# Performance work log

Measured on AMD Instinct MI355X. Metric: run time of the kernel, lower is better.

The kernel has to match this reference:

```python
import jax, jax.numpy as jnp
import numpy as np

EPS = 1e-6
N_HEADS = 16
N_KV_HEADS = 4
HEAD_DIM = 128
DIM = 2048
SEQ = 2048
BATCH = 2


def _make_freqs_cis(seqlen, head_dim, theta=10000.0):
    inv = 1.0 / (theta ** (jnp.arange(0, head_dim, 2, dtype=jnp.float32) / head_dim))  # [hd/2]
    t = jnp.arange(seqlen, dtype=jnp.float32)
    ang = jnp.outer(t, inv)  # [seq, hd/2]
    return jnp.stack([jnp.cos(ang), jnp.sin(ang)], axis=-1)  # [seq, hd/2, 2]


def setup_inputs() -> dict:
    key = jax.random.key(0)
    k1, k2, k3 = jax.random.split(key, 3)
    std = 0.02
    x = jax.random.normal(k1, (BATCH, SEQ, DIM), dtype=jnp.float32)
    freqs_cis = _make_freqs_cis(SEQ, HEAD_DIM)
    norm_w = jnp.ones((DIM,), dtype=jnp.float32)
    wqkv_w = jax.random.normal(k2, ((N_HEADS + 2 * N_KV_HEADS) * HEAD_DIM, DIM), dtype=jnp.float32) * std
    wo_w = jax.random.normal(k3, (DIM, N_HEADS * HEAD_DIM), dtype=jnp.float32) * std
    return {"x": x, "freqs_cis": freqs_cis, "norm_w": norm_w, "wqkv_w": wqkv_w, "wo_w": wo_w}


def _rope(t, cos, sin):
    # t: [b, s, h, hd] viewed as pairs; cos/sin: [s, hd/2]
    b, s, h, hd = t.shape
    tr = t.reshape(b, s, h, hd // 2, 2)
    xr, xi = tr[..., 0], tr[..., 1]
    c = cos[None, :, None, :]
    sn = sin[None, :, None, :]
    out_r = xr * c - xi * sn
    out_i = xr * sn + xi * c
    return jnp.stack([out_r, out_i], axis=-1).reshape(b, s, h, hd)


def reference(x, freqs_cis, norm_w, wqkv_w, wo_w):
    bs, seqlen, dim = x.shape
    n_rep = N_HEADS // N_KV_HEADS
    # RMSNorm
    xn = x * jax.lax.rsqrt(jnp.mean(x * x, axis=-1, keepdims=True) + EPS) * norm_w
    # fused QKV projection
    qkv = jnp.einsum('bsd,ed->bse', xn, wqkv_w)
    q_sz = N_HEADS * HEAD_DIM
    kv_sz = N_KV_HEADS * HEAD_DIM
    xq = qkv[..., :q_sz].reshape(bs, seqlen, N_HEADS, HEAD_DIM)
    xk = qkv[..., q_sz:q_sz + kv_sz].reshape(bs, seqlen, N_KV_HEADS, HEAD_DIM)
    xv = qkv[..., q_sz + kv_sz:].reshape(bs, seqlen, N_KV_HEADS, HEAD_DIM)
    cos, sin = freqs_cis[..., 0], freqs_cis[..., 1]
    xq = _rope(xq, cos, sin)
    xk = _rope(xk, cos, sin)
    # GQA: group q heads so kv broadcast replaces repeat_kv materialization
    q = xq.transpose(0, 2, 1, 3).reshape(bs, N_KV_HEADS, n_rep, seqlen, HEAD_DIM)
    k = xk.transpose(0, 2, 1, 3)  # [b, g, s, d]
    v = xv.transpose(0, 2, 1, 3)
    scale = 1.0 / jnp.sqrt(jnp.float32(HEAD_DIM))
    scores = jnp.einsum('bgrqd,bgkd->bgrqk', q, k) * scale
    causal = jnp.tril(jnp.ones((seqlen, seqlen), dtype=bool))
    scores = jnp.where(causal, scores, jnp.finfo(scores.dtype).min)
    probs = jax.nn.softmax(scores, axis=-1)
    out = jnp.einsum('bgrqk,bgkd->bgrqd', probs, v)
    out = out.reshape(bs, N_HEADS, seqlen, HEAD_DIM).transpose(0, 2, 1, 3).reshape(bs, seqlen, N_HEADS * HEAD_DIM)
    return jnp.einsum('bse,de->bsd', out, wo_w)
```

## Files before the change

### kernel.cpp

```cpp
#include <hip/hip_runtime.h>
#include <cstdint>
#include <cstddef>

typedef __bf16 bhalf;
typedef __bf16 bhalf8 __attribute__((ext_vector_type(8)));
typedef __bf16 bhalf4 __attribute__((ext_vector_type(4)));
typedef float f32x4 __attribute__((ext_vector_type(4)));
typedef float f32x16 __attribute__((ext_vector_type(16)));

#define RMS_EPS 1e-6f
#define N_HEADS 16
#define N_KV 4
#define HD 128
#define DIM 2048
#define SEQ 2048
#define BATCH 2

static __device__ __forceinline__ f32x4 mfma16(bhalf8 a, bhalf8 b, f32x4 c) {
    return __builtin_amdgcn_mfma_f32_16x16x32_bf16(a, b, c, 0, 0, 0);
}
static __device__ __forceinline__ f32x16 mfma32(bhalf8 a, bhalf8 b, f32x16 c) {
    return __builtin_amdgcn_mfma_f32_32x32x16_bf16(a, b, c, 0, 0, 0);
}

static __device__ __forceinline__ void gload16(const bhalf* g, bhalf* l) {
    __builtin_amdgcn_global_load_lds((const __attribute__((address_space(1))) unsigned int*)g,
                                     (__attribute__((address_space(3))) unsigned int*)l,
                                     16, 0, 0);
}

static __device__ __forceinline__ unsigned cvt_pk_bf16(float a, float b) {
    unsigned r;
    asm volatile("v_cvt_pk_bf16_f32 %0, %1, %2" : "=v"(r) : "v"(a), "v"(b));
    return r;
}
static __device__ __forceinline__ void plane32_swap(unsigned& a, unsigned& b) {
    asm volatile("v_permlane32_swap_b32 %0, %1" : "+v"(a), "+v"(b));
}

__global__ __launch_bounds__(256) void cvt_w(const float* __restrict__ a,
                                             const float* __restrict__ b,
                                             bhalf* __restrict__ dst) {
    size_t i = ((size_t)blockIdx.x * 256 + threadIdx.x) * 4;
    const size_t NQ = (size_t)3072 * 2048;
    float4 v = (i < NQ) ? ((const float4*)a)[i >> 2] : ((const float4*)b)[(i - NQ) >> 2];
    bhalf4 o;
    o[0] = (bhalf)v.x; o[1] = (bhalf)v.y; o[2] = (bhalf)v.z; o[3] = (bhalf)v.w;
    *(bhalf4*)(dst + i) = o;
}

__global__ __launch_bounds__(256) void rmsnorm_k(const float* __restrict__ x,
                                                 const float* __restrict__ w,
                                                 bhalf* __restrict__ xn) {
    const int row = blockIdx.x;
    const int tid = threadIdx.x;
    const float4* xr = (const float4*)(x + (size_t)row * DIM);
    float4 v0 = xr[tid * 2], v1 = xr[tid * 2 + 1];
    float ss = v0.x * v0.x + v0.y * v0.y + v0.z * v0.z + v0.w * v0.w
             + v1.x * v1.x + v1.y * v1.y + v1.z * v1.z + v1.w * v1.w;
    #pragma unroll
    for (int off = 32; off; off >>= 1) ss += __shfl_xor(ss, off, 64);
    __shared__ float red[4];
    if ((tid & 63) == 0) red[tid >> 6] = ss;
    __syncthreads();
    float tot = red[0] + red[1] + red[2] + red[3];
    float scale = rsqrtf(tot * (1.0f / DIM) + RMS_EPS);
    const float4* wr = (const float4*)w;
    float4 w0 = wr[tid * 2], w1 = wr[tid * 2 + 1];
    bhalf8 o;
    o[0] = (bhalf)(v0.x * scale * w0.x); o[1] = (bhalf)(v0.y * scale * w0.y);
    o[2] = (bhalf)(v0.z * scale * w0.z); o[3] = (bhalf)(v0.w * scale * w0.w);
    o[4] = (bhalf)(v1.x * scale * w1.x); o[5] = (bhalf)(v1.y * scale * w1.y);
    o[6] = (bhalf)(v1.z * scale * w1.z); o[7] = (bhalf)(v1.w * scale * w1.w);
    *(bhalf8*)(xn + (size_t)row * DIM + tid * 8) = o;
}

template <typename OutT>
__global__ __launch_bounds__(512) void gemm256(const bhalf* __restrict__ A,
                                               const bhalf* __restrict__ B,
                                               OutT* __restrict__ C,
                                               int N, int K) {
    extern __shared__ __align__(16) char smem[];
    const int tid = threadIdx.x;
    const int wid = tid >> 6, lane = tid & 63;
    const int quad = lane >> 4, r16 = lane & 15;
    const int wm = wid >> 2, wn = wid & 3;

    const int nx = N >> 8;
    const int cpx = (int)gridDim.x >> 3;
    const int bs = (int)blockIdx.x;
    const int bid = (bs & 7) * cpx + (bs >> 3);
    const int m0 = (bid / nx) << 8, n0 = (bid % nx) << 8;

    const int srow = wid * 32 + (lane >> 2);
    const int scol = ((lane & 3) ^ ((lane >> 2) & 3)) << 3;
    const bhalf* Ast = A + (size_t)(m0 + srow) * K + scol;
    const bhalf* Bst = B + (size_t)(n0 + srow) * K + scol;
    const size_t r16K = (size_t)16 * K;

    const int xorr = (r16 & 3) << 4;
    const int rdA = (wm * 128 + r16) * 64 + ((quad * 16) ^ xorr);
    const int rdB = (wn * 64 + r16) * 64 + ((quad * 16) ^ xorr);

    char* const sA = smem;
    char* const sB = smem + 49152;

    f32x4 acc[8][4];
    #pragma unroll
    for (int i = 0; i < 8; ++i)
        #pragma unroll
        for (int j = 0; j < 4; ++j) acc[i][j] = (f32x4)0.0f;

    const int NT = K >> 5;

    #define STAGE256(P, bufbase, t) do {                                          \
        gload16((P) + (size_t)(t) * 32, (bhalf*)((bufbase) + wid * 2048));        \
        gload16((P) + (size_t)(t) * 32 + r16K, (bhalf*)((bufbase) + wid * 2048 + 1024)); \
    } while (0)

    STAGE256(Ast, sA, 0);
    STAGE256(Bst, sB, 0);
    STAGE256(Ast, sA + 16384, 1);
    STAGE256(Bst, sB + 16384, 1);
    asm volatile("s_waitcnt vmcnt(4)" ::: "memory");
    __builtin_amdgcn_s_barrier();

    int cur = 0, c2 = 2;
    for (int t = 0; t < NT; ++t) {
        char* const bufA = sA + cur * 16384;
        char* const bufB = sB + cur * 16384;
        bhalf8 bf[4], afl[4];
        #pragma unroll
        for (int j = 0; j < 4; ++j) bf[j] = *(const bhalf8*)(bufB + rdB + j * 1024);
        #pragma unroll
        for (int i = 0; i < 4; ++i) afl[i] = *(const bhalf8*)(bufA + rdA + i * 1024);
        if (t + 2 < NT) STAGE256(Ast, sA + c2 * 16384, t + 2);
        __builtin_amdgcn_s_barrier();
        __builtin_amdgcn_s_setprio(1);
        #pragma unroll
        for (int i = 0; i < 4; ++i)
            #pragma unroll
            for (int j = 0; j < 4; ++j)
                acc[i][j] = mfma16(afl[i], bf[j], acc[i][j]);
        __builtin_amdgcn_s_setprio(0);
        __builtin_amdgcn_s_barrier();
        bhalf8 afh[4];
        #pragma unroll
        for (int i = 0; i < 4; ++i) afh[i] = *(const bhalf8*)(bufA + rdA + 4096 + i * 1024);
        if (t + 2 < NT) STAGE256(Bst, sB + c2 * 16384, t + 2);
        asm volatile("s_waitcnt vmcnt(4)" ::: "memory");
        __builtin_amdgcn_s_barrier();
        __builtin_amdgcn_s_setprio(1);
        #pragma unroll
        for (int i = 0; i < 4; ++i)
            #pragma unroll
            for (int j = 0; j < 4; ++j)
                acc[i + 4][j] = mfma16(afh[i], bf[j], acc[i + 4][j]);
        __builtin_amdgcn_s_setprio(0);
        __builtin_amdgcn_s_barrier();
        cur = (cur == 2) ? 0 : cur + 1;
        c2 = (c2 == 2) ? 0 : c2 + 1;
    }
    #undef STAGE256

    #pragma unroll
    for (int i = 0; i < 8; ++i) {
        const int rbase = m0 + wm * 128 + i * 16 + quad * 4;
        #pragma unroll
        for (int rr = 0; rr < 4; ++rr) {
            OutT* crow = C + (size_t)(rbase + rr) * N + n0 + wn * 64 + r16;
            #pragma unroll
            for (int j = 0; j < 4; ++j) crow[j * 16] = (OutT)acc[i][j][rr];
        }
    }
}

__global__ __launch_bounds__(256) void rope_k(const bhalf* __restrict__ qkv,
                                              const float* __restrict__ freqs,
                                              bhalf* __restrict__ qb,
                                              bhalf* __restrict__ kb,
                                              bhalf* __restrict__ vt) {
    const int bs = blockIdx.x;
    const int b = bs >> 11, s = bs & 2047;
    const bhalf* row = qkv + (size_t)bs * 3072;
    const int tid = threadIdx.x;

    {
        const int h = tid >> 4, d20 = (tid & 15) * 4;
        bhalf8 e = *(const bhalf8*)(row + h * HD + d20 * 2);
        const float* fp = freqs + (size_t)s * 128 + d20 * 2;
        float4 f0 = *(const float4*)fp;
        float4 f1 = *(const float4*)(fp + 4);
        bhalf8 o;
        o[0] = (bhalf)((float)e[0] * f0.x - (float)e[1] * f0.y);
        o[1] = (bhalf)((float)e[0] * f0.y + (float)e[1] * f0.x);
        o[2] = (bhalf)((float)e[2] * f0.z - (float)e[3] * f0.w);
        o[3] = (bhalf)((float)e[2] * f0.w + (float)e[3] * f0.z);
        o[4] = (bhalf)((float)e[4] * f1.x - (float)e[5] * f1.y);
        o[5] = (bhalf)((float)e[4] * f1.y + (float)e[5] * f1.x);
        o[6] = (bhalf)((float)e[6] * f1.z - (float)e[7] * f1.w);
        o[7] = (bhalf)((float)e[6] * f1.w + (float)e[7] * f1.z);
        *(bhalf8*)(qb + ((size_t)(b * N_HEADS + h) * SEQ + s) * HD + d20 * 2) = o;
    }
    if (tid < 64) {
        const int kh = tid >> 4, d20 = (tid & 15) * 4;
        bhalf8 e = *(const bhalf8*)(row + 2048 + kh * HD + d20 * 2);
        const float* fp = freqs + (size_t)s * 128 + d20 * 2;
        float4 f0 = *(const float4*)fp;
        float4 f1 = *(const float4*)(fp + 4);
        bhalf8 o;
        o[0] = (bhalf)((float)e[0] * f0.x - (float)e[1] * f0.y);
        o[1] = (bhalf)((float)e[0] * f0.y + (float)e[1] * f0.x);
        o[2] = (bhalf)((float)e[2] * f0.z - (float)e[3] * f0.w);
        o[3] = (bhalf)((float)e[2] * f0.w + (float)e[3] * f0.z);
        o[4] = (bhalf)((float)e[4] * f1.x - (float)e[5] * f1.y);
        o[5] = (bhalf)((float)e[4] * f1.y + (float)e[5] * f1.x);
        o[6] = (bhalf)((float)e[6] * f1.z - (float)e[7] * f1.w);
        o[7] = (bhalf)((float)e[6] * f1.w + (float)e[7] * f1.z);
        *(bhalf8*)(kb + ((size_t)(b * N_KV + kh) * SEQ + s) * HD + d20 * 2) = o;
    }
    for (int e = tid; e < 512; e += 256) {
        const int kh = e >> 7, d = e & 127;
        vt[((size_t)(b * N_KV + kh) * HD + d) * SEQ + s] = row[2560 + e];
    }
}

__global__ __launch_bounds__(256, 2) void attn_k(const bhalf* __restrict__ qb,
                                                 const bhalf* __restrict__ kb,
                                                 const bhalf* __restrict__ vt,
                                                 bhalf* __restrict__ ob) {
    const int tid = threadIdx.x;
    const int wave = tid >> 6, lane = tid & 63;
    const int l31 = lane & 31, h2 = lane >> 5;
    const int qw = wave & 1, kw = wave >> 1;
    const int bid = ((blockIdx.x & 7) << 6) | ((int)blockIdx.x >> 3);
    const int pair = bid & 15;
    const int hh = (bid >> 4) & 15;
    const int b = bid >> 8;
    const int kvh = hh >> 2;

    __shared__ __align__(16) char smem[33792];
    char* const sK = smem;
    char* const sV = smem + 16384;
    float* const mrg = (float*)smem;

    const bhalf* Kbase = kb + (size_t)(b * N_KV + kvh) * SEQ * HD;
    const bhalf* Vbase = vt + (size_t)(b * N_KV + kvh) * HD * SEQ;
    const float SCL2 = 0.08838834764831845f * 1.4426950408889634f;

    const int mbase = (qw * 64 + lane) * 66;
    const int kr = tid >> 4, kce = (tid & 15) * 8;
    const int vr = tid >> 3, vce = (tid & 7) * 8;
    const int kcB = kce * 2, vcB = vce * 2;
    const int Xl = (h2 << 4) ^ ((l31 & 7) << 4);

    for (int phase = 0; phase < 2; ++phase) {
        const int qt = phase ? (31 - pair) : pair;
        const int qrow = qt * 64 + qw * 32 + l31;
        const int qhi = qt * 64 + qw * 32 + 31;

        const bhalf* qbase = qb + (((size_t)(b * N_HEADS + hh) * SEQ) + qrow) * HD;
        bhalf8 qf[8];
        #pragma unroll
        for (int kk = 0; kk < 8; ++kk) {
            bhalf8 q0 = *(const bhalf8*)(qbase + kk * 16 + h2 * 8);
            #pragma unroll
            for (int e = 0; e < 8; ++e) q0[e] = (bhalf)((float)q0[e] * SCL2);
            qf[kk] = q0;
        }

        f32x16 accO[4];
        #pragma unroll
        for (int dt = 0; dt < 4; ++dt) accO[dt] = (f32x16)0.0f;
        float m_i = -1e30f, l_i = 0.0f;

        bhalf8 kreg[4], vreg[4];
        #pragma unroll
        for (int i = 0; i < 4; ++i) {
            kreg[i] = *(const bhalf8*)(Kbase + (size_t)(kr + 16 * i) * HD + kce);
            vreg[i] = *(const bhalf8*)(Vbase + (size_t)(vr + 32 * i) * SEQ + vce);
        }

        for (int kt = 0; kt <= qt; ++kt) {
            __syncthreads();
            #pragma unroll
            for (int i = 0; i < 4; ++i) {
                const int rk = kr + 16 * i;
                *(bhalf8*)(sK + rk * 256 + (kcB ^ ((rk & 7) << 4))) = kreg[i];
                const int rv = vr + 32 * i;
                *(bhalf8*)(sV + rv * 128 + (vcB ^ ((rv & 7) << 4))) = vreg[i];
            }
            __syncthreads();
            if (kt < qt) {
                const int kn = (kt + 1) * 64;
                #pragma unroll
                for (int i = 0; i < 4; ++i) {
                    kreg[i] = *(const bhalf8*)(Kbase + (size_t)(kn + kr + 16 * i) * HD + kce);
                    vreg[i] = *(const bhalf8*)(Vbase + (size_t)(vr + 32 * i) * SEQ + kn + vce);
                }
            }
            if (qhi < kt * 64 + kw * 32) continue;

            f32x16 accS = (f32x16)0.0f;
            const char* kRow = sK + (kw * 32 + l31) * 256;
            #pragma unroll
            for (int kk = 0; kk < 8; ++kk)
                accS = mfma32(*(const bhalf8*)(kRow + ((kk * 32) ^ Xl)), qf[kk], accS);

            if (kt == qt) {
                #pragma unroll
                for (int r = 0; r < 16; ++r) {
                    const int key = kt * 64 + kw * 32 + (r & 3) + 8 * (r >> 2) + 4 * h2;
                    if (key > qrow) accS[r] = -1e30f;
                }
            }

            float mx = -1e30f;
            #pragma unroll
            for (int r = 0; r < 16; ++r) mx = fmaxf(mx, accS[r]);
            mx = fmaxf(mx, __shfl_xor(mx, 32, 64));

            if (!__all(mx <= m_i + 8.0f)) {
                const float mnew = fmaxf(m_i, mx);
                const float alpha = __builtin_amdgcn_exp2f(m_i - mnew);
                m_i = mnew;
                l_i *= alpha;
                #pragma unroll
                for (int dt = 0; dt < 4; ++dt)
                    #pragma unroll
                    for (int r = 0; r < 16; ++r) accO[dt][r] *= alpha;
            }

            float p[16];
            float rs = 0.0f;
            #pragma unroll
            for (int r = 0; r < 16; ++r) {
                p[r] = __builtin_amdgcn_exp2f(accS[r] - m_i);
                rs += p[r];
            }
            rs += __shfl_xor(rs, 32, 64);
            l_i += rs;

            unsigned X0 = cvt_pk_bf16(p[0],  p[1]);
            unsigned X1 = cvt_pk_bf16(p[2],  p[3]);
            unsigned X2 = cvt_pk_bf16(p[4],  p[5]);
            unsigned X3 = cvt_pk_bf16(p[6],  p[7]);
            unsigned X4 = cvt_pk_bf16(p[8],  p[9]);
            unsigned X5 = cvt_pk_bf16(p[10], p[11]);
            unsigned X6 = cvt_pk_bf16(p[12], p[13]);
            unsigned X7 = cvt_pk_bf16(p[14], p[15]);
            plane32_swap(X0, X2);
            plane32_swap(X1, X3);
            plane32_swap(X4, X6);
            plane32_swap(X5, X7);
            union { unsigned u[8]; bhalf8 h[2]; } pk;
            pk.u[0] = X0; pk.u[1] = X1; pk.u[2] = X2; pk.u[3] = X3;
            pk.u[4] = X4; pk.u[5] = X5; pk.u[6] = X6; pk.u[7] = X7;

            #pragma unroll
            for (int kk2 = 0; kk2 < 2; ++kk2) {
                const int cb = (kw << 6) | (kk2 << 5);
                #pragma unroll
                for (int dt = 0; dt < 4; ++dt) {
                    const bhalf8 vfv = *(const bhalf8*)(sV + (dt * 32 + l31) * 128 + (cb ^ Xl));
                    accO[dt] = mfma32(vfv, pk.h[kk2], accO[dt]);
                }
            }
        }

        __syncthreads();
        if (kw == 1) {
            #pragma unroll
            for (int dt = 0; dt < 4; ++dt)
                #pragma unroll
                for (int r = 0; r < 16; ++r) mrg[mbase + dt * 16 + r] = accO[dt][r];
            mrg[mbase + 64] = m_i;
            mrg[mbase + 65] = l_i;
        }
        __syncthreads();
        if (kw == 0) {
            const float m1 = mrg[mbase + 64];
            const float l1 = mrg[mbase + 65];
            const float m = fmaxf(m_i, m1);
            const float b0 = __builtin_amdgcn_exp2f(m_i - m);
            const float b1 = __builtin_amdgcn_exp2f(m1 - m);
            const float inv = 1.0f / (l_i * b0 + l1 * b1);
            bhalf* obase = ob + ((size_t)b * SEQ + qrow) * (size_t)(N_HEADS * HD) + hh * HD;
            #pragma unroll
            for (int dt = 0; dt < 4; ++dt)
                #pragma unroll
                for (int c = 0; c < 4; ++c) {
                    bhalf4 o4;
                    #pragma unroll
                    for (int rr = 0; rr < 4; ++rr) {
                        const float v = accO[dt][c * 4 + rr] * b0 +
                                        mrg[mbase + dt * 16 + c * 4 + rr] * b1;
                        o4[rr] = (bhalf)(v * inv);
                    }
                    *(bhalf4*)(obase + dt * 32 + c * 8 + h2 * 4) = o4;
                }
        }
    }
}

extern "C" void kernel_launch(void* const* d_in, const int* in_sizes, int n_in,
                              void* d_out, int out_size, void* d_ws, size_t ws_size,
                              hipStream_t stream) {
    const float* x      = (const float*)d_in[0];
    const float* freqs  = (const float*)d_in[1];
    const float* norm_w = (const float*)d_in[2];
    const float* wqkv   = (const float*)d_in[3];
    const float* wo     = (const float*)d_in[4];
    float* out = (float*)d_out;

    char* ws = (char*)d_ws;
    bhalf* wqkv_b = (bhalf*)(ws);
    bhalf* wo_b   = (bhalf*)(ws + 12582912);
    bhalf* xn     = (bhalf*)(ws + 20971520);
    bhalf* qkv    = (bhalf*)(ws + 37748736);
    bhalf* qb     = (bhalf*)(ws + 88080384);
    bhalf* kb     = (bhalf*)(ws + 104857600);
    bhalf* vtb    = (bhalf*)(ws + 109051904);
    bhalf* attn   = (bhalf*)(ws + 113246208);

    static bool attr_done = false;
    if (!attr_done) {
        hipFuncSetAttribute((const void*)gemm256<bhalf>,
                            hipFuncAttributeMaxDynamicSharedMemorySize, 98304);
        hipFuncSetAttribute((const void*)gemm256<float>,
                            hipFuncAttributeMaxDynamicSharedMemorySize, 98304);
        attr_done = true;
    }

    cvt_w<<<10240, 256, 0, stream>>>(wqkv, wo, wqkv_b);
    rmsnorm_k<<<BATCH * SEQ, 256, 0, stream>>>(x, norm_w, xn);
    gemm256<bhalf><<<192, 512, 98304, stream>>>(xn, wqkv_b, qkv, 3072, 2048);
    rope_k<<<BATCH * SEQ, 256, 0, stream>>>(qkv, freqs, qb, kb, vtb);
    attn_k<<<512, 256, 0, stream>>>(qb, kb, vtb, attn);
    gemm256<float><<<128, 512, 98304, stream>>>(attn, wo_b, out, 2048, 2048);
}
```

Before: 323.6 us.

## Rewrite GEMM mainloop as 8-phase pipeline with K=64 tiles and double buffering

Replaces the 256x256 GEMM mainloop with K=64 tiles split into quarter-tile stages that are interleaved across eight MFMA phases per buffer, using a two-buffer 128KB LDS layout with an 8-wide XOR swizzle. Each phase issues one global-to-LDS stage between barrier-separated MFMA bursts, so there are more barriers but each burst is shorter. The aim is better overlap of global loads, LDS reads and MFMA work, and fewer LDS bank conflicts, in both the QKV and output projections. The larger LDS footprint and the added barriers could limit occupancy or add synchronisation stalls.

Result: faster. 316.1 us (-2.3%).

```diff
diff --git a/kernel.cpp b/kernel.cpp
--- a/kernel.cpp
+++ b/kernel.cpp
@@ -76,10 +76,10 @@
 }
 
 template <typename OutT>
-__global__ __launch_bounds__(512) void gemm256(const bhalf* __restrict__ A,
-                                               const bhalf* __restrict__ B,
-                                               OutT* __restrict__ C,
-                                               int N, int K) {
+__global__ __launch_bounds__(512) void gemm8p(const bhalf* __restrict__ A,
+                                              const bhalf* __restrict__ B,
+                                              OutT* __restrict__ C,
+                                              int N, int K) {
     extern __shared__ __align__(16) char smem[];
     const int tid = threadIdx.x;
     const int wid = tid >> 6, lane = tid & 63;
@@ -92,18 +92,19 @@
     const int bid = (bs & 7) * cpx + (bs >> 3);
     const int m0 = (bid / nx) << 8, n0 = (bid % nx) << 8;
 
-    const int srow = wid * 32 + (lane >> 2);
-    const int scol = ((lane & 3) ^ ((lane >> 2) & 3)) << 3;
-    const bhalf* Ast = A + (size_t)(m0 + srow) * K + scol;
-    const bhalf* Bst = B + (size_t)(n0 + srow) * K + scol;
-    const size_t r16K = (size_t)16 * K;
-
-    const int xorr = (r16 & 3) << 4;
-    const int rdA = (wm * 128 + r16) * 64 + ((quad * 16) ^ xorr);
-    const int rdB = (wn * 64 + r16) * 64 + ((quad * 16) ^ xorr);
-
-    char* const sA = smem;
-    char* const sB = smem + 49152;
+    const int srow = wid * 8 + (lane >> 3);
+    const int scol = ((lane & 7) ^ ((lane >> 3) & 7)) << 3;
+    const bhalf* Asrc = A + (size_t)(m0 + srow) * K + scol;
+    const bhalf* Bsrc = B + (size_t)(n0 + srow) * K + scol;
+    const size_t r64K = (size_t)64 * K;
+    const size_t r128K = (size_t)128 * K;
+
+    const int x7 = r16 & 7;
+    const int sl0 = (quad ^ (x7 & 3)) << 4;
+    const int ksx = (x7 >> 2) << 6;
+    const int k0 = ksx, k1 = 64 ^ ksx;
+    const int aoff = (wm << 14) + (r16 << 7) + sl0;
+    const int boff = ((2 + (wn >> 1)) << 14) + ((((wn & 1) << 6) + r16) << 7) + sl0;
 
     f32x4 acc[8][4];
     #pragma unroll
@@ -111,57 +112,106 @@
         #pragma unroll
         for (int j = 0; j < 4; ++j) acc[i][j] = (f32x4)0.0f;
 
-    const int NT = K >> 5;
-
-    #define STAGE256(P, bufbase, t) do {                                          \
-        gload16((P) + (size_t)(t) * 32, (bhalf*)((bufbase) + wid * 2048));        \
-        gload16((P) + (size_t)(t) * 32 + r16K, (bhalf*)((bufbase) + wid * 2048 + 1024)); \
-    } while (0)
-
-    STAGE256(Ast, sA, 0);
-    STAGE256(Bst, sB, 0);
-    STAGE256(Ast, sA + 16384, 1);
-    STAGE256(Bst, sB + 16384, 1);
-    asm volatile("s_waitcnt vmcnt(4)" ::: "memory");
+    const int NT = K >> 6;
+    const int H = K >> 4;
+    int h = 8;
+
+    auto STAGE = [&](int hidx) {
+        const int T = hidx >> 2, f = hidx & 3;
+        const bhalf* s = ((f < 2) ? Asrc : Bsrc) + ((f & 1) ? r128K : 0) + T * 64;
+        char* d = smem + ((T & 1) << 16) + (f << 14) + (wid << 10);
+        gload16(s, (bhalf*)d);
+        gload16(s + r64K, (bhalf*)(d + 8192));
+    };
+
+    #pragma unroll
+    for (int i = 0; i < 8; ++i) STAGE(i);
+    asm volatile("s_waitcnt vmcnt(8)" ::: "memory");
     __builtin_amdgcn_s_barrier();
 
-    int cur = 0, c2 = 2;
-    for (int t = 0; t < NT; ++t) {
-        char* const bufA = sA + cur * 16384;
-        char* const bufB = sB + cur * 16384;
-        bhalf8 bf[4], afl[4];
-        #pragma unroll
-        for (int j = 0; j < 4; ++j) bf[j] = *(const bhalf8*)(bufB + rdB + j * 1024);
-        #pragma unroll
-        for (int i = 0; i < 4; ++i) afl[i] = *(const bhalf8*)(bufA + rdA + i * 1024);
-        if (t + 2 < NT) STAGE256(Ast, sA + c2 * 16384, t + 2);
-        __builtin_amdgcn_s_barrier();
-        __builtin_amdgcn_s_setprio(1);
-        #pragma unroll
-        for (int i = 0; i < 4; ++i)
-            #pragma unroll
-            for (int j = 0; j < 4; ++j)
-                acc[i][j] = mfma16(afl[i], bf[j], acc[i][j]);
-        __builtin_amdgcn_s_setprio(0);
-        __builtin_amdgcn_s_barrier();
-        bhalf8 afh[4];
-        #pragma unroll
-        for (int i = 0; i < 4; ++i) afh[i] = *(const bhalf8*)(bufA + rdA + 4096 + i * 1024);
-        if (t + 2 < NT) STAGE256(Bst, sB + c2 * 16384, t + 2);
-        asm volatile("s_waitcnt vmcnt(4)" ::: "memory");
-        __builtin_amdgcn_s_barrier();
-        __builtin_amdgcn_s_setprio(1);
-        #pragma unroll
-        for (int i = 0; i < 4; ++i)
-            #pragma unroll
-            for (int j = 0; j < 4; ++j)
-                acc[i + 4][j] = mfma16(afh[i], bf[j], acc[i + 4][j]);
-        __builtin_amdgcn_s_setprio(0);
-        __builtin_amdgcn_s_barrier();
-        cur = (cur == 2) ? 0 : cur + 1;
-        c2 = (c2 == 2) ? 0 : c2 + 1;
-    }
-    #undef STAGE256
+    bhalf8 af[4][2], bf[4][2];
+
+    for (int t = 0; t < NT; t += 2) {
+        #pragma unroll
+        for (int hf = 0; hf < 2; ++hf) {
+            char* const bp = smem + (hf << 16);
+            #pragma unroll
+            for (int i = 0; i < 4; ++i) {
+                af[i][0] = *(const bhalf8*)(bp + aoff + i * 2048 + k0);
+                af[i][1] = *(const bhalf8*)(bp + aoff + i * 2048 + k1);
+            }
+            #pragma unroll
+            for (int j = 0; j < 2; ++j) {
+                bf[j][0] = *(const bhalf8*)(bp + boff + j * 2048 + k0);
+                bf[j][1] = *(const bhalf8*)(bp + boff + j * 2048 + k1);
+            }
+            if ((t > 0 || hf == 1) && h < H) STAGE(h++);
+            asm volatile("s_waitcnt lgkmcnt(8)" ::: "memory");
+            __builtin_amdgcn_s_barrier();
+            __builtin_amdgcn_s_setprio(1);
+            #pragma unroll
+            for (int i = 0; i < 4; ++i)
+                #pragma unroll
+                for (int j = 0; j < 2; ++j) {
+                    acc[i][j] = mfma16(af[i][0], bf[j][0], acc[i][j]);
+                    acc[i][j] = mfma16(af[i][1], bf[j][1], acc[i][j]);
+                }
+            __builtin_amdgcn_s_setprio(0);
+            __builtin_amdgcn_s_barrier();
+
+            #pragma unroll
+            for (int j = 2; j < 4; ++j) {
+                bf[j][0] = *(const bhalf8*)(bp + boff + j * 2048 + k0);
+                bf[j][1] = *(const bhalf8*)(bp + boff + j * 2048 + k1);
+            }
+            if ((t > 0 || hf == 1) && h < H) STAGE(h++);
+            __builtin_amdgcn_s_barrier();
+            __builtin_amdgcn_s_setprio(1);
+            #pragma unroll
+            for (int i = 0; i < 4; ++i)
+                #pragma unroll
+                for (int j = 2; j < 4; ++j) {
+                    acc[i][j] = mfma16(af[i][0], bf[j][0], acc[i][j]);
+                    acc[i][j] = mfma16(af[i][1], bf[j][1], acc[i][j]);
+                }
+            __builtin_amdgcn_s_setprio(0);
+            __builtin_amdgcn_s_barrier();
+
+            #pragma unroll
+            for (int i = 0; i < 4; ++i) {
+                af[i][0] = *(const bhalf8*)(bp + aoff + (i + 4) * 2048 + k0);
+                af[i][1] = *(const bhalf8*)(bp + aoff + (i + 4) * 2048 + k1);
+            }
+            if ((t > 0 || hf == 1) && h < H) STAGE(h++);
+            __builtin_amdgcn_s_barrier();
+            __builtin_amdgcn_s_setprio(1);
+            #pragma unroll
+            for (int i = 0; i < 4; ++i)
+                #pragma unroll
+                for (int j = 0; j < 2; ++j) {
+                    acc[i + 4][j] = mfma16(af[i][0], bf[j][0], acc[i + 4][j]);
+                    acc[i + 4][j] = mfma16(af[i][1], bf[j][1], acc[i + 4][j]);
+                }
+            __builtin_amdgcn_s_setprio(0);
+            __builtin_amdgcn_s_barrier();
+
+            bool st = (h < H);
+            if (st) STAGE(h++);
+            __builtin_amdgcn_s_barrier();
+            __builtin_amdgcn_s_setprio(1);
+            #pragma unroll
+            for (int i = 0; i < 4; ++i)
+                #pragma unroll
+                for (int j = 2; j < 4; ++j) {
+                    acc[i + 4][j] = mfma16(af[i][0], bf[j][0], acc[i + 4][j]);
+                    acc[i + 4][j] = mfma16(af[i][1], bf[j][1], acc[i + 4][j]);
+                }
+            __builtin_amdgcn_s_setprio(0);
+            if (st) asm volatile("s_waitcnt vmcnt(2)" ::: "memory");
+            else    asm volatile("s_waitcnt vmcnt(0)" ::: "memory");
+            __builtin_amdgcn_s_barrier();
+        }
+    }
 
     #pragma unroll
     for (int i = 0; i < 8; ++i) {
@@ -425,17 +475,17 @@
 
     static bool attr_done = false;
     if (!attr_done) {
-        hipFuncSetAttribute((const void*)gemm256<bhalf>,
-                            hipFuncAttributeMaxDynamicSharedMemorySize, 98304);
-        hipFuncSetAttribute((const void*)gemm256<float>,
-                            hipFuncAttributeMaxDynamicSharedMemorySize, 98304);
+        hipFuncSetAttribute((const void*)gemm8p<bhalf>,
+                            hipFuncAttributeMaxDynamicSharedMemorySize, 131072);
+        hipFuncSetAttribute((const void*)gemm8p<float>,
+                            hipFuncAttributeMaxDynamicSharedMemorySize, 131072);
         attr_done = true;
     }
 
     cvt_w<<<10240, 256, 0, stream>>>(wqkv, wo, wqkv_b);
     rmsnorm_k<<<BATCH * SEQ, 256, 0, stream>>>(x, norm_w, xn);
-    gemm256<bhalf><<<192, 512, 98304, stream>>>(xn, wqkv_b, qkv, 3072, 2048);
+    gemm8p<bhalf><<<192, 512, 131072, stream>>>(xn, wqkv_b, qkv, 3072, 2048);
     rope_k<<<BATCH * SEQ, 256, 0, stream>>>(qkv, freqs, qb, kb, vtb);
     attn_k<<<512, 256, 0, stream>>>(qb, kb, vtb, attn);
-    gemm256<float><<<128, 512, 98304, stream>>>(attn, wo_b, out, 2048, 2048);
-}
+    gemm8p<float><<<128, 512, 131072, stream>>>(attn, wo_b, out, 2048, 2048);
+}
```
